# Kernel optimization log

Hardware: AMD Instinct MI355X
Metric: run time of the kernel (lower is better)

Reference implementation:

```python
import jax, jax.numpy as jnp
import numpy as np

THR = 0.2
POOL_A = 160
POOL_B = 96
EPS = 1e-5


def _adaptive_avg_pool_last(x, out_size):
    # torch AdaptiveAvgPool1d semantics: bin i averages [floor(i*n/o), ceil((i+1)*n/o))
    n = x.shape[-1]
    i = np.arange(out_size)
    starts = (i * n) // out_size
    ends = -((-(i + 1) * n) // out_size)
    cs = jnp.cumsum(x, axis=-1)
    cs = jnp.concatenate([jnp.zeros_like(cs[..., :1]), cs], axis=-1)
    sums = cs[..., ends] - cs[..., starts]
    return sums / jnp.asarray(ends - starts, x.dtype)


def _unfold3x3(x, H, W):
    # Faithful to torch: raw reshape (N, L, C) -> (N, C, H, W) (memory reinterpretation,
    # NOT a transpose), then F.unfold(k=3, pad=1) and rearrange 'n (c ww) l -> n l ww c'.
    N, L, C = x.shape
    img = x.reshape(N, C, H, W)
    pad = jnp.pad(img, ((0, 0), (0, 0), (1, 1), (1, 1)))
    # window positions in row-major (ky, kx) order, matching F.unfold
    patches = jnp.stack([pad[:, :, dy:dy + H, dx:dx + W]
                         for dy in range(3) for dx in range(3)], axis=2)  # (N,C,9,H,W)
    return patches.transpose(0, 3, 4, 2, 1).reshape(N, H * W, 9, C)  # (N,L,9,C)


def _forward(feat_s0, feat_s1, ln_weight, ln_bias):
    N, L, C = feat_s0.shape
    H = W = int(round(L ** 0.5))
    conf = jnp.einsum('nlc,nsc->nls', feat_s0, feat_s1) / (C ** 0.5)
    conf = jax.nn.softmax(conf, axis=1) * jax.nn.softmax(conf, axis=2)
    # mutual nearest-neighbor mask with confidence threshold
    mask = ((conf > THR)
            & (conf == conf.max(axis=2, keepdims=True))
            & (conf == conf.max(axis=1, keepdims=True))).astype(feat_s0.dtype)
    u0 = _unfold3x3(feat_s0, H, W)
    u1 = _unfold3x3(feat_s1, H, W)
    sem0 = jnp.einsum('nlc,nlwc->nlw', feat_s0, u0) / C  # divided by C (shape[-1]), as in source
    sem1 = jnp.einsum('nlc,nlwc->nlw', feat_s1, u1) / C
    fea0 = jnp.einsum('nlwc,nlw->nlc', u0, sem0)
    fea1 = jnp.einsum('nlwc,nlw->nlc', u1, sem1)
    s0 = jnp.einsum('nls,nsd->nld', mask, fea1) / L
    s1 = jnp.einsum('nsl,nsd->nld', mask, fea0) / L
    f0 = jnp.concatenate([_adaptive_avg_pool_last(feat_s0, POOL_A),
                          _adaptive_avg_pool_last(s0, POOL_B)], axis=-1)
    f1 = jnp.concatenate([_adaptive_avg_pool_last(feat_s1, POOL_A),
                          _adaptive_avg_pool_last(s1, POOL_B)], axis=-1)
    f = jnp.concatenate([f0, f1], axis=0)  # (2N, L, 256)
    mu = f.mean(-1, keepdims=True)
    var = f.var(-1, keepdims=True)
    f = (f - mu) * jax.lax.rsqrt(var + EPS) * ln_weight + ln_bias
    return f[:N], f[N:]


def setup_inputs():
    key = jax.random.key(0)
    k0, k1 = jax.random.split(key)
    N, L, C = 2, 4096, 256
    return {
        'feat_s0': jax.random.normal(k0, (N, L, C), jnp.float32),
        'feat_s1': jax.random.normal(k1, (N, L, C), jnp.float32),
        'ln_weight': jnp.ones((C,), jnp.float32),
        'ln_bias': jnp.zeros((C,), jnp.float32),
    }


def reference(feat_s0, feat_s1, ln_weight, ln_bias):
    return _forward(feat_s0, feat_s1, ln_weight, ln_bias)
```

## Files before the change

### kernel.cpp

```cpp
#include <hip/hip_runtime.h>
#include <stdint.h>

#define NBATCH 2
#define LL 4096
#define CC 256
#define KEXP 0.09016844f
#define KEXP2 0.18033688f
#define IMIN (-2147483647 - 1)

typedef long i64f;
typedef float f32x4 __attribute__((ext_vector_type(4)));

#if defined(__has_builtin) && __has_builtin(__builtin_amdgcn_exp2f)
#define EXP2F(x) __builtin_amdgcn_exp2f(x)
#else
#define EXP2F(x) exp2f(x)
#endif

#define GLDS16(g, l) __builtin_amdgcn_global_load_lds(                      \
    (const __attribute__((address_space(1))) uint32_t*)(g),                 \
    (__attribute__((address_space(3))) uint32_t*)(l), 16, 0, 0)

__global__ __launch_bounds__(256) void cast_fp8(
    const float* __restrict__ a, const float* __restrict__ b,
    uint32_t* __restrict__ oa, uint32_t* __restrict__ ob,
    float* __restrict__ rowSum, float* __restrict__ colSum,
    int* __restrict__ rowPart, int* __restrict__ colPart){
  int idx = blockIdx.x * 256 + threadIdx.x;
  if (idx < NBATCH*LL){
    rowSum[idx] = 0.f; colSum[idx] = 0.f;
    rowPart[idx] = IMIN; colPart[idx] = IMIN;
  }
  float4 va = ((const float4*)a)[idx];
  float4 vb = ((const float4*)b)[idx];
  int ra = __builtin_amdgcn_cvt_pk_fp8_f32(va.x, va.y, 0, false);
  ra = __builtin_amdgcn_cvt_pk_fp8_f32(va.z, va.w, ra, true);
  int rb = __builtin_amdgcn_cvt_pk_fp8_f32(vb.x, vb.y, 0, false);
  rb = __builtin_amdgcn_cvt_pk_fp8_f32(vb.z, vb.w, rb, true);
  oa[idx] = (uint32_t)ra;
  ob[idx] = (uint32_t)rb;
}

__global__ __launch_bounds__(256, 4) void conf_pass(
    const uint8_t* __restrict__ f0q, const uint8_t* __restrict__ f1q,
    float* __restrict__ rowSum, float* __restrict__ colSum,
    int* __restrict__ rowPart, int* __restrict__ colPart){
  __shared__ __align__(16) uint8_t Alds[128*128];
  __shared__ __align__(16) uint8_t Blds[128*128];
  float* rowS = (float*)Alds;
  float* colS = (float*)(Alds + 1024);
  int*   rb   = (int*)  (Alds + 2048);
  int*   cb   = (int*)  (Alds + 3072);
  int bl = (blockIdx.z*32 + blockIdx.y)*32 + blockIdx.x;
  int nb = (bl & 7)*256 + (bl >> 3);
  int st = nb & 31, lt = (nb >> 5) & 31, n = nb >> 10;
  int t = threadIdx.x;
  const int wv = t >> 6, lane = t & 63, lr = lane & 15, quad = lane >> 4;
  const int lq = wv >> 1, sq = wv & 1;
  const int swzr = (lr & 7) << 4;
  const uint8_t* A = f0q + (size_t)n*LL*CC + (size_t)(lt*128)*CC;
  const uint8_t* B = f1q + (size_t)n*LL*CC + (size_t)(st*128)*CC;
  f32x4 acc[4][4];
  #pragma unroll
  for (int r = 0; r < 4; r++)
    #pragma unroll
    for (int j = 0; j < 4; j++) acc[r][j] = (f32x4){0.f,0.f,0.f,0.f};

  auto compute = [&](){
    __builtin_amdgcn_s_setprio(1);
    #pragma unroll
    for (int kk = 0; kk < 4; kk++){
      int off = (kk*32 + quad*8) ^ swzr;
      i64f a[4], bf[4];
      #pragma unroll
      for (int r = 0; r < 4; r++)
        a[r] = *(const i64f*)(Alds + (lq*64 + r*16 + lr)*128 + off);
      #pragma unroll
      for (int j = 0; j < 4; j++)
        bf[j] = *(const i64f*)(Blds + (sq*64 + j*16 + lr)*128 + off);
      #pragma unroll
      for (int r = 0; r < 4; r++)
        #pragma unroll
        for (int j = 0; j < 4; j++)
          acc[r][j] = __builtin_amdgcn_mfma_f32_16x16x32_fp8_fp8(a[r], bf[j], acc[r][j], 0, 0, 0);
    }
    __builtin_amdgcn_s_setprio(0);
  };

  {
    int rsub = lane >> 3, csub = lane & 7;
    int srcOff = ((csub ^ rsub) << 4);
    #pragma unroll
    for (int m = 0; m < 4; m++){
      int row = m*32 + wv*8 + rsub;
      GLDS16(A + (size_t)row*CC + srcOff, Alds + m*4096 + wv*1024);
      GLDS16(B + (size_t)row*CC + srcOff, Blds + m*4096 + wv*1024);
    }
  }
  __builtin_amdgcn_sched_barrier(0);
  uint2 pa[8], pb[8];
  #pragma unroll
  for (int m = 0; m < 8; m++){
    int f = m*256 + t, row = f >> 4, kg = f & 15;
    int so = (kg*8) ^ ((row & 7) << 4);
    pa[m] = *(const uint2*)(A + (size_t)row*CC + 128 + so);
    pb[m] = *(const uint2*)(B + (size_t)row*CC + 128 + so);
  }
  asm volatile("s_waitcnt vmcnt(16)" ::: "memory");
  __builtin_amdgcn_s_barrier();
  __builtin_amdgcn_sched_barrier(0);
  compute();
  __syncthreads();
  #pragma unroll
  for (int m = 0; m < 8; m++){
    int f = m*256 + t, row = f >> 4, kg = f & 15;
    *(uint2*)(Alds + row*128 + kg*8) = pa[m];
    *(uint2*)(Blds + row*128 + kg*8) = pb[m];
  }
  __syncthreads();
  compute();

  const int sbase = st*128 + sq*64 + lr;
  const int lbase = lt*128 + lq*64 + quad*4;
  float rv[16], cv[4] = {0.f,0.f,0.f,0.f};
  int rk[16], ck[4] = {IMIN,IMIN,IMIN,IMIN};
  #pragma unroll
  for (int i = 0; i < 16; i++){ rv[i] = 0.f; rk[i] = IMIN; }
  #pragma unroll
  for (int r = 0; r < 4; r++)
    #pragma unroll
    for (int j = 0; j < 4; j++)
      #pragma unroll
      for (int rr = 0; rr < 4; rr++){
        float a = acc[r][j][rr];
        float e = EXP2F(a * KEXP);
        rv[r*4+rr] += e;
        cv[j] += e;
        int iqs = ((int)(a * 2048.f)) << 12;
        rk[r*4+rr] = max(rk[r*4+rr], iqs + (sbase + j*16));
        ck[j]      = max(ck[j],      iqs + (lbase + r*16 + rr));
      }
  {
    bool hi = (lr & 1) != 0;
    #pragma unroll
    for (int i = 0; i < 8; i++){
      float sf = hi ? rv[i] : rv[i+8], kf = hi ? rv[i+8] : rv[i];
      rv[i] = kf + __shfl_xor(sf, 1);
      int   si = hi ? rk[i] : rk[i+8]; int ki = hi ? rk[i+8] : rk[i];
      rk[i] = max(ki, __shfl_xor(si, 1));
    }
  }
  {
    bool hi = (lr & 2) != 0;
    #pragma unroll
    for (int i = 0; i < 4; i++){
      float sf = hi ? rv[i] : rv[i+4], kf = hi ? rv[i+4] : rv[i];
      rv[i] = kf + __shfl_xor(sf, 2);
      int   si = hi ? rk[i] : rk[i+4]; int ki = hi ? rk[i+4] : rk[i];
      rk[i] = max(ki, __shfl_xor(si, 2));
    }
  }
  {
    bool hi = (lr & 4) != 0;
    #pragma unroll
    for (int i = 0; i < 2; i++){
      float sf = hi ? rv[i] : rv[i+2], kf = hi ? rv[i+2] : rv[i];
      rv[i] = kf + __shfl_xor(sf, 4);
      int   si = hi ? rk[i] : rk[i+2]; int ki = hi ? rk[i+2] : rk[i];
      rk[i] = max(ki, __shfl_xor(si, 4));
    }
  }
  {
    bool hi = (lr & 8) != 0;
    float sf = hi ? rv[0] : rv[1], kf = hi ? rv[1] : rv[0];
    rv[0] = kf + __shfl_xor(sf, 8);
    int   si = hi ? rk[0] : rk[1]; int ki = hi ? rk[1] : rk[0];
    rk[0] = max(ki, __shfl_xor(si, 8));
  }
  {
    bool hi = (lane & 16) != 0;
    #pragma unroll
    for (int i = 0; i < 2; i++){
      float sf = hi ? cv[i] : cv[i+2], kf = hi ? cv[i+2] : cv[i];
      cv[i] = kf + __shfl_xor(sf, 16);
      int   si = hi ? ck[i] : ck[i+2]; int ki = hi ? ck[i+2] : ck[i];
      ck[i] = max(ki, __shfl_xor(si, 16));
    }
  }
  {
    bool hi = (lane & 32) != 0;
    float sf = hi ? cv[0] : cv[1], kf = hi ? cv[1] : cv[0];
    cv[0] = kf + __shfl_xor(sf, 32);
    int   si = hi ? ck[0] : ck[1]; int ki = hi ? ck[1] : ck[0];
    ck[0] = max(ki, __shfl_xor(si, 32));
  }
  const int V = ((lr&1)<<3) | ((lr&2)<<1) | ((lr&4)>>1) | ((lr&8)>>3);
  const int J = ((quad&1)<<1) | (quad>>1);
  const int rowOwn = lq*64 + (V>>2)*16 + quad*4 + (V&3);
  const int colOwn = sq*64 + J*16 + lr;
  __syncthreads();
  rowS[sq*128 + rowOwn] = rv[0];
  rb  [sq*128 + rowOwn] = rk[0];
  colS[lq*128 + colOwn] = cv[0];
  cb  [lq*128 + colOwn] = ck[0];
  __syncthreads();
  {
    int tt = t & 127;
    if (t < 128){
      unsafeAtomicAdd(&rowSum[(size_t)n*LL + lt*128 + tt], rowS[tt] + rowS[128 + tt]);
      atomicMax(&rowPart[(size_t)n*LL + lt*128 + tt], max(rb[tt], rb[128 + tt]));
    } else {
      unsafeAtomicAdd(&colSum[(size_t)n*LL + st*128 + tt], colS[tt] + colS[128 + tt]);
      atomicMax(&colPart[(size_t)n*LL + st*128 + tt], max(cb[tt], cb[128 + tt]));
    }
  }
}

__device__ float fea_fly(const float* __restrict__ featn, int srow, int t){
  __shared__ float sred[9][4];
  __shared__ float ssem[9];
  int lane = t & 63, wv = t >> 6;
  int h = srow >> 6, xx = srow & 63;
  float fv = featn[(size_t)srow * CC + t];
  float uv[9];
  #pragma unroll
  for (int w = 0; w < 9; w++){
    int dy = w/3 - 1, dx = w%3 - 1;
    int y = h + dy, x = xx + dx;
    uv[w] = (y >= 0 && y < 64 && x >= 0 && x < 64) ? featn[(size_t)t * 4096 + y*64 + x] : 0.f;
  }
  __syncthreads();
  #pragma unroll
  for (int w = 0; w < 9; w++){
    float pvv = fv * uv[w];
    #pragma unroll
    for (int msk = 1; msk <= 32; msk <<= 1) pvv += __shfl_xor(pvv, msk);
    if (lane == 0) sred[w][wv] = pvv;
  }
  __syncthreads();
  if (t < 9) ssem[t] = (sred[t][0] + sred[t][1] + sred[t][2] + sred[t][3]) * (1.f/256.f);
  __syncthreads();
  float acc = 0.f;
  #pragma unroll
  for (int w = 0; w < 9; w++) acc += uv[w] * ssem[w];
  __syncthreads();
  return acc;
}

__device__ __forceinline__ float pool_window(const float* f, const float* s, int t){
  if (t < 160){
    int a = (t*8)/5, e = (t*8+12)/5;
    float sum = 0.f;
    for (int i = a; i < e; i++) sum += f[i];
    return sum / (float)(e - a);
  } else {
    int tt = t - 160;
    int a = (tt*8)/3, e = (tt*8+10)/3;
    float sum = 0.f;
    for (int i = a; i < e; i++) sum += s[i];
    return sum / (float)(e - a);
  }
}

__global__ __launch_bounds__(256) void tail(
    const float* __restrict__ feat0, const float* __restrict__ feat1,
    const float* __restrict__ rowSum, const float* __restrict__ colSum,
    const int* __restrict__ rowPart, const int* __restrict__ colPart,
    const float* __restrict__ lnw, const float* __restrict__ lnb,
    float* __restrict__ out){
  int l0 = blockIdx.x * 4, n = blockIdx.y, t = threadIdx.x;
  int lane = t & 63, wv = t >> 6;
  size_t base = (size_t)n * LL;
  float w = lnw[t], bsh = lnb[t];
  float fv0[4], fv1[4], Rl[4], Cl[4];
  int rowK[4], colK[4];
  #pragma unroll
  for (int i = 0; i < 4; i++){
    fv0[i]  = feat0[(base + l0 + i)*CC + t];
    fv1[i]  = feat1[(base + l0 + i)*CC + t];
    rowK[i] = rowPart[base + l0 + i];
    colK[i] = colPart[base + l0 + i];
    Rl[i]   = rowSum[base + l0 + i];
    Cl[i]   = colSum[base + l0 + i];
  }
  int ssr[4], ssc[4], ck2[4], rk2[4];
  float Cssr[4], Rssc[4];
  #pragma unroll
  for (int i = 0; i < 4; i++){
    ssr[i] = rowK[i] & 4095;
    ssc[i] = colK[i] & 4095;
    Cssr[i] = colSum[base + ssr[i]];
    Rssc[i] = rowSum[base + ssc[i]];
    ck2[i]  = colPart[base + ssr[i]];
    rk2[i]  = rowPart[base + ssc[i]];
  }
  __shared__ float f0r[CC], f1r[CC], s0r[CC], s1r[CC];
  __shared__ float redA[2][4], redB[2][4];
  for (int i = 0; i < 4; i++){
    int l = l0 + i;
    float v0 = 0.f, v1 = 0.f;
    {
      float araw = (float)(rowK[i] >> 12) * (1.f/2048.f);
      float val = exp2f(araw * KEXP2) / (Rl[i] * Cssr[i]);
      if (val > 0.2f && (ck2[i] & 4095) == l)
        v0 = fea_fly(feat1 + (size_t)n*LL*CC, ssr[i], t) * (1.f/4096.f);
    }
    {
      float araw = (float)(colK[i] >> 12) * (1.f/2048.f);
      float val = exp2f(araw * KEXP2) / (Cl[i] * Rssc[i]);
      if (val > 0.2f && (rk2[i] & 4095) == l)
        v1 = fea_fly(feat0 + (size_t)n*LL*CC, ssc[i], t) * (1.f/4096.f);
    }
    f0r[t] = fv0[i];
    f1r[t] = fv1[i];
    s0r[t] = v0;
    s1r[t] = v1;
    __syncthreads();
    float pA = pool_window(f0r, s0r, t);
    float pB = pool_window(f1r, s1r, t);
    float smA = pA, sqA = pA*pA, smB = pB, sqB = pB*pB;
    #pragma unroll
    for (int msk = 1; msk <= 32; msk <<= 1){
      smA += __shfl_xor(smA, msk);
      sqA += __shfl_xor(sqA, msk);
      smB += __shfl_xor(smB, msk);
      sqB += __shfl_xor(sqB, msk);
    }
    if (lane == 0){ redA[0][wv] = smA; redA[1][wv] = sqA; redB[0][wv] = smB; redB[1][wv] = sqB; }
    __syncthreads();
    float tsA = redA[0][0]+redA[0][1]+redA[0][2]+redA[0][3];
    float tqA = redA[1][0]+redA[1][1]+redA[1][2]+redA[1][3];
    float tsB = redB[0][0]+redB[0][1]+redB[0][2]+redB[0][3];
    float tqB = redB[1][0]+redB[1][1]+redB[1][2]+redB[1][3];
    float muA = tsA * (1.f/256.f), varA = tqA * (1.f/256.f) - muA*muA;
    float muB = tsB * (1.f/256.f), varB = tqB * (1.f/256.f) - muB*muB;
    out[((size_t)n*LL + l)*CC + t]       = (pA - muA) * rsqrtf(varA + 1e-5f) * w + bsh;
    out[((size_t)(2 + n)*LL + l)*CC + t] = (pB - muB) * rsqrtf(varB + 1e-5f) * w + bsh;
    __syncthreads();
  }
}

extern "C" void kernel_launch(void* const* d_in, const int* in_sizes, int n_in,
                              void* d_out, int out_size, void* d_ws, size_t ws_size,
                              hipStream_t stream){
  const float* feat0 = (const float*)d_in[0];
  const float* feat1 = (const float*)d_in[1];
  const float* lnw   = (const float*)d_in[2];
  const float* lnb   = (const float*)d_in[3];
  float* out = (float*)d_out;
  char* ws = (char*)d_ws;
  const size_t MB = 1024 * 1024;
  uint8_t* f0q = (uint8_t*)(ws + 0);
  uint8_t* f1q = (uint8_t*)(ws + 2*MB);
  float* rowSum  = (float*)(ws + 4*MB);
  float* colSum  = (float*)(ws + 4*MB + 32*1024);
  int*   rowPart = (int*)  (ws + 4*MB + 64*1024);
  int*   colPart = (int*)  (ws + 4*MB + 96*1024);

  cast_fp8<<<2048, 256, 0, stream>>>(feat0, feat1, (uint32_t*)f0q, (uint32_t*)f1q,
                                     rowSum, colSum, rowPart, colPart);
  dim3 gconf(32, 32, NBATCH);
  conf_pass<<<gconf, 256, 0, stream>>>(f0q, f1q, rowSum, colSum, rowPart, colPart);
  dim3 gt(LL/4, NBATCH);
  tail<<<gt, 256, 0, stream>>>(feat0, feat1, rowSum, colSum, rowPart, colPart,
                               lnw, lnb, out);
}
```

Measured before the change: 117.7 us.

## Use scaled 16x16x128 FP8 MFMA and simplify the K-chunk staging

Swaps the 16x16x32 FP8 MFMA loop for the gfx950 scaled 16x16x128 f8f6f4 MFMA with unit scales, so each 128-wide K chunk needs one instruction per output tile instead of four. Operands are now read as two 16-byte LDS loads per row. Staging changes as well: the register-prefetch path for the second K chunk is dropped, and both chunks go through direct global-to-LDS loads with barriers in between. This removes the overlap between loading the second chunk and computing the first, and correctness depends on the swizzle matching the new operand layout.

```diff
diff --git a/kernel.cpp b/kernel.cpp
--- a/kernel.cpp
+++ b/kernel.cpp
@@ -7,9 +7,10 @@
 #define KEXP 0.09016844f
 #define KEXP2 0.18033688f
 #define IMIN (-2147483647 - 1)
-
-typedef long i64f;
+#define SCL1 0x7F7F7F7Fu
+
 typedef float f32x4 __attribute__((ext_vector_type(4)));
+typedef int   i32x8 __attribute__((ext_vector_type(8)));
 
 #if defined(__has_builtin) && __has_builtin(__builtin_amdgcn_exp2f)
 #define EXP2F(x) __builtin_amdgcn_exp2f(x)
@@ -66,59 +67,50 @@
     #pragma unroll
     for (int j = 0; j < 4; j++) acc[r][j] = (f32x4){0.f,0.f,0.f,0.f};
 
-  auto compute = [&](){
-    __builtin_amdgcn_s_setprio(1);
-    #pragma unroll
-    for (int kk = 0; kk < 4; kk++){
-      int off = (kk*32 + quad*8) ^ swzr;
-      i64f a[4], bf[4];
-      #pragma unroll
-      for (int r = 0; r < 4; r++)
-        a[r] = *(const i64f*)(Alds + (lq*64 + r*16 + lr)*128 + off);
-      #pragma unroll
-      for (int j = 0; j < 4; j++)
-        bf[j] = *(const i64f*)(Blds + (sq*64 + j*16 + lr)*128 + off);
-      #pragma unroll
-      for (int r = 0; r < 4; r++)
-        #pragma unroll
-        for (int j = 0; j < 4; j++)
-          acc[r][j] = __builtin_amdgcn_mfma_f32_16x16x32_fp8_fp8(a[r], bf[j], acc[r][j], 0, 0, 0);
-    }
-    __builtin_amdgcn_s_setprio(0);
-  };
-
-  {
+  auto stage = [&](int kc){
     int rsub = lane >> 3, csub = lane & 7;
-    int srcOff = ((csub ^ rsub) << 4);
+    int srcOff = kc*128 + ((csub ^ rsub) << 4);
     #pragma unroll
     for (int m = 0; m < 4; m++){
       int row = m*32 + wv*8 + rsub;
       GLDS16(A + (size_t)row*CC + srcOff, Alds + m*4096 + wv*1024);
       GLDS16(B + (size_t)row*CC + srcOff, Blds + m*4096 + wv*1024);
     }
-  }
-  __builtin_amdgcn_sched_barrier(0);
-  uint2 pa[8], pb[8];
-  #pragma unroll
-  for (int m = 0; m < 8; m++){
-    int f = m*256 + t, row = f >> 4, kg = f & 15;
-    int so = (kg*8) ^ ((row & 7) << 4);
-    pa[m] = *(const uint2*)(A + (size_t)row*CC + 128 + so);
-    pb[m] = *(const uint2*)(B + (size_t)row*CC + 128 + so);
-  }
-  asm volatile("s_waitcnt vmcnt(16)" ::: "memory");
-  __builtin_amdgcn_s_barrier();
-  __builtin_amdgcn_sched_barrier(0);
-  compute();
-  __syncthreads();
-  #pragma unroll
-  for (int m = 0; m < 8; m++){
-    int f = m*256 + t, row = f >> 4, kg = f & 15;
-    *(uint2*)(Alds + row*128 + kg*8) = pa[m];
-    *(uint2*)(Blds + row*128 + kg*8) = pb[m];
-  }
-  __syncthreads();
-  compute();
+  };
+
+  auto computeS = [&](){
+    __builtin_amdgcn_s_setprio(1);
+    i32x8 af[4];
+    #pragma unroll
+    for (int r = 0; r < 4; r++){
+      const uint8_t* base = Alds + (lq*64 + r*16 + lr)*128;
+      uint4 lo = *(const uint4*)(base + ((quad*32)      ^ swzr));
+      uint4 hi = *(const uint4*)(base + ((quad*32 + 16) ^ swzr));
+      af[r] = (i32x8){(int)lo.x,(int)lo.y,(int)lo.z,(int)lo.w,
+                      (int)hi.x,(int)hi.y,(int)hi.z,(int)hi.w};
+    }
+    #pragma unroll
+    for (int j = 0; j < 4; j++){
+      const uint8_t* base = Blds + (sq*64 + j*16 + lr)*128;
+      uint4 lo = *(const uint4*)(base + ((quad*32)      ^ swzr));
+      uint4 hi = *(const uint4*)(base + ((quad*32 + 16) ^ swzr));
+      i32x8 bf = (i32x8){(int)lo.x,(int)lo.y,(int)lo.z,(int)lo.w,
+                         (int)hi.x,(int)hi.y,(int)hi.z,(int)hi.w};
+      #pragma unroll
+      for (int r = 0; r < 4; r++)
+        acc[r][j] = __builtin_amdgcn_mfma_scale_f32_16x16x128_f8f6f4(
+            af[r], bf, acc[r][j], 0, 0, 0, SCL1, 0, SCL1);
+    }
+    __builtin_amdgcn_s_setprio(0);
+  };
+
+  stage(0);
+  __syncthreads();
+  computeS();
+  __syncthreads();
+  stage(1);
+  __syncthreads();
+  computeS();
 
   const int sbase = st*128 + sq*64 + lr;
   const int lbase = lt*128 + lq*64 + quad*4;
```

New measurement: 118.2 us. No clear change (+0.4%).
